# Kernel tuning notes

Measured on AMD Instinct MI355X. Metric: run time of the kernel, lower is better.

## Reference

```python
import jax, jax.numpy as jnp
import numpy as np

R = 2                                   # NMS radius (init kwarg r)
EPS = float(np.finfo(np.float32).eps)   # torch.finfo(float32).eps
PI = float(np.pi)


def _sobel(x):
    """Kornia SpatialGradient (sobel, normalized): x [N,1,H,W] -> (dx, dy) each [N,1,H,W]."""
    kx = jnp.array([[-1., 0., 1.], [-2., 0., 2.], [-1., 0., 1.]], jnp.float32) / 8.0
    ky = kx.T
    k = jnp.stack([kx, ky])[:, None]    # [2,1,3,3] -> out channels dx, dy
    xp = jnp.pad(x, ((0, 0), (0, 0), (1, 1), (1, 1)), mode='edge')  # replicate pad
    out = jax.lax.conv_general_dilated(xp, k, (1, 1), 'VALID',
                                       dimension_numbers=('NCHW', 'OIHW', 'NCHW'))
    return out[:, 0:1], out[:, 1:2]


def _theta(mask):
    """Edge direction from one-hot mask, per STEAL edges_nms. mask [N,1,H,W]."""
    dx, dy = _sobel(mask)
    gxx, _ = _sobel(dx)
    gxy, gyy = _sobel(dy)
    return jnp.fmod(jnp.arctan(gyy * jnp.sign(-gxy + EPS) / (gxx + EPS)), PI)


def setup_inputs() -> dict:
    key = jax.random.key(0)
    k1, k2 = jax.random.split(key)
    pred_labels = jax.random.normal(k1, (4, 16, 512, 1024), dtype=jnp.float32)
    true_labels = jax.random.randint(k2, (4, 512, 1024), 0, 16, dtype=jnp.int64)
    return {"pred_labels": pred_labels, "true_labels": true_labels}


def reference(pred_labels, true_labels):
    B, C, H, W = pred_labels.shape
    # per-class one-hot masks -> direction maps
    onehot = jax.nn.one_hot(true_labels, C, dtype=jnp.float32)        # [B,H,W,C]
    masks = onehot.transpose(0, 3, 1, 2).reshape(B * C, 1, H, W)
    theta = _theta(masks).reshape(B, C, H, W)
    thresh_theta = jnp.fmod(jnp.round(theta * (5.0 / PI)) + 5.0, 5.0)  # {0..4}
    dirs = jnp.fmod(thresh_theta, 4.0).astype(jnp.int32)               # {0,1,2,3}

    exp_p = jnp.exp(pred_labels)
    js = list(range(-R, R))
    # offsets (dx_off, dy_off) summed in the denominator for each direction
    offs = {
        0: [(0, j) for j in js],        # horizontal: preds[x, y-r:y+r]
        1: [(j, -j - 1) for j in js],   # anti-diagonal
        2: [(j, 0) for j in js],        # vertical: preds[x-r:x+r, y]
        3: [(-j - 1, j) for j in js],   # anti-diagonal (reversed traversal, same set)
    }
    denom = jnp.ones_like(exp_p)
    for d in range(4):
        dd = exp_p * 0.0
        for ox, oy in offs[d]:
            dd = dd + jnp.roll(exp_p, (-ox, -oy), axis=(2, 3))  # exp_p[x+ox, y+oy]
        denom = jnp.where(dirs == d, dd, denom)

    interior = jnp.zeros((H, W), bool).at[R:H - R, R:W - R].set(True)
    nms = jnp.where(interior, exp_p / denom, 0.0)
    return jnp.sum(nms)
```

## Files before the change

### kernel.cpp

```cpp
#include <hip/hip_runtime.h>


#define Bn 4
#define Cn 16
#define Hn 512
#define Wn 1024

typedef unsigned long long u64;
typedef unsigned int u32;
typedef float f4u __attribute__((ext_vector_type(4), aligned(4)));
typedef int   i4u __attribute__((ext_vector_type(4), aligned(4)));

static __device__ __forceinline__ float fast_rcp(float x) {
#if __has_builtin(__builtin_amdgcn_rcpf)
  return __builtin_amdgcn_rcpf(x);
#else
  return 1.0f / x;
#endif
}


#define P1TW 128
#define P1TH 8
#define P1LW 132
#define P1LH 12

__global__ __launch_bounds__(256)
void dir_kernel(const int* __restrict__ labels, u32* __restrict__ dirs)
{
  __shared__ unsigned char labt[P1LH][P1LW];

  const int w0 = blockIdx.x * P1TW;
  const int h0 = blockIdx.y * P1TH;
  const int b  = blockIdx.z;
  const int tid = threadIdx.x;

  const int* lbase = labels + (size_t)b * (Hn*Wn);
  const bool interior = (h0 >= 2) && (h0 + P1TH + 2 <= Hn) &&
                        (w0 >= 2) && (w0 + P1TW + 2 <= Wn);
  if (interior) {
    const int* lb = lbase + (size_t)(h0-2)*Wn + (w0-2);
    for (int i = tid; i < P1LH*33; i += 256) {
      int row = i / 33, c4 = (i - row*33) * 4;
      i4u L = *(const i4u*)(lb + row*Wn + c4);
      *(u32*)&labt[row][c4] =
          (u32)L.x | ((u32)L.y << 8) | ((u32)L.z << 16) | ((u32)L.w << 24);
    }
  } else {
    for (int i = tid; i < P1LH*33; i += 256) {
      int row = i / 33, c4 = (i - row*33) * 4;
      int gh = min(max(h0-2+row, 0), Hn-1);
      const int* lr = lbase + gh*Wn;
      u32 v = 0;
      #pragma unroll
      for (int k = 0; k < 4; ++k) {
        int gw = min(max(w0-2+c4+k, 0), Wn-1);
        v |= (u32)(lr[gw] & 0xff) << (8*k);
      }
      *(u32*)&labt[row][c4] = v;
    }
  }
  __syncthreads();

  const int tcol = tid & 31;
  const int trow = tid >> 5;

  u64 W[5];
  #pragma unroll
  for (int r = 0; r < 5; ++r) {
    const u32* lp = (const u32*)&labt[trow + r][0];
    u64 lo = lp[tcol];
    u64 hi = lp[tcol + 1];
    W[r] = lo | (hi << 32);
  }

  u32 pack[4] = {0u, 0u, 0u, 0u};

  #pragma unroll 1
  for (int c = 0; c < 16; ++c) {
    const u64 crep = 0x0101010101010101ULL * (u32)c;
    u64 m[5];
    #pragma unroll
    for (int r = 0; r < 5; ++r) {
      u64 x = W[r] ^ crep;
      m[r] = ((0x8080808080808080ULL - x) & 0x8080808080808080ULL) >> 7;
    }
    u64 t  = m[1] + m[3];
    u64 VA = m[0] + m[4] + (t << 2) + (m[2] << 2) + (m[2] << 1);
    u64 VB = ((m[3] << 1) + m[4] + 0x0303030303030303ULL)
             - (m[0] + (m[1] << 1));
    u64 VC = (m[0] + m[4] + 0x0202020202020202ULL) - (m[2] << 1);
    u64 gxxp = (VA + (VA >> 32) + 0x4040404040404040ULL) - ((VA >> 16) << 1);
    u64 q1   = (VC >> 8) + (VC >> 24);
    u64 w16  = VC >> 16;
    u64 gyyp = (VC + (VC >> 32)) + (q1 << 2) + (w16 << 2) + (w16 << 1);
    u64 gxyp = (((VB >> 24) << 1) + (VB >> 32) + 0x2020202020202020ULL)
             - (VB + ((VB >> 8) << 1));

    u32 gxxl = (u32)gxxp, gyyl = (u32)gyyp, gxyl = (u32)gxyp;
    #pragma unroll
    for (int k = 0; k < 4; ++k) {
      int gxx = (int)((gxxl >> (8*k)) & 0xffu) - 64;
      int gyy = (int)((gyyl >> (8*k)) & 0xffu) - 32;
      int gxyb = (int)((gxyl >> (8*k)) & 0xffu);
      int ax = gxx < 0 ? -gxx : gxx;
      int ay = gyy < 0 ? -gyy : gyy;
      int t1 = (ay * 100  > ax * 33)   ? 1 : 0;
      int t2 = (ay * 1000 > ax * 1377) ? 1 : 0;
      int rb = t1 + t2;
      bool ng = ((gyy < 0) != (gxyb > 32)) != (gxx < 0);
      int dir = ng ? ((rb == 2) ? 3 : 0) : rb;
      pack[k] |= (u32)dir << (2*c);
    }
  }

  const int gh = h0 + trow;
  u32* drow = dirs + ((size_t)b*Hn + gh)*Wn + (w0 + 4*tcol);
  *(uint4*)drow = make_uint4(pack[0], pack[1], pack[2], pack[3]);
}


#define TW 128
#define TH 16
#define LW 132
#define LH 20
#define NT 256

__global__ __launch_bounds__(NT)
void nms_sum_kernel(const float* __restrict__ pred,
                    const u32* __restrict__ dirs,
                    float* __restrict__ slots)
{
  __shared__ float ext[LH][LW];
  __shared__ float wsum[NT/64];

  const int w0 = blockIdx.x * TW;
  const int h0 = blockIdx.y * TH;
  const int bz = blockIdx.z;
  const int b  = bz >> 4;
  const int c  = bz & 15;
  const int tid = threadIdx.x;

  const int lane = tid & 63;
  const int wq   = tid >> 6;
  const int hr0  = wq * 4;
  const int gw0  = w0 + 2*lane;

  u64 dp[4];
  {
    const u32* dbase = dirs + (size_t)b*Hn*Wn;
    #pragma unroll
    for (int i = 0; i < 4; ++i) {
      int gh = h0 + hr0 + i;
      dp[i] = *(const u64*)(dbase + (size_t)gh*Wn + gw0);
    }
  }

  const float* plane = pred + (size_t)(b*Cn + c) * (size_t)(Hn*Wn);
  const bool interior = (h0 >= 2) && (h0 + TH + 2 <= Hn) &&
                        (w0 >= 2) && (w0 + TW + 2 <= Wn);
  if (interior) {
    const float* pb = plane + (size_t)(h0-2)*Wn + (w0-2);
    for (int i = tid; i < LH*33; i += NT) {
      int row = i / 33, c4 = (i - row*33) * 4;
      f4u p = *(const f4u*)(pb + row*Wn + c4);
      float4 e;
      e.x = __expf(p.x); e.y = __expf(p.y); e.z = __expf(p.z); e.w = __expf(p.w);
      *(float4*)&ext[row][c4] = e;
    }
  } else {
    for (int i = tid; i < LH*(LW/2); i += NT) {
      int row = i / (LW/2);
      int col = (i - row*(LW/2)) * 2;
      int gh = min(max(h0-2+row, 0), Hn-1);
      int ga = min(max(w0-2+col,   0), Wn-1);
      int gb = min(max(w0-1+col,   0), Wn-1);
      const float* prow = plane + gh*Wn;
      *(float2*)&ext[row][col] = make_float2(__expf(prow[ga]), __expf(prow[gb]));
    }
  }
  __syncthreads();

  const bool wvalid0 = (gw0     >= 2) && (gw0     < Wn-2);
  const bool wvalid1 = (gw0 + 1 >= 2) && (gw0 + 1 < Wn-2);
  const u32 sh = 2u * (u32)c;

  float acc = 0.f;

  float exr[4][5];
  const int fb = 2*lane;
  #pragma unroll
  for (int r = 0; r < 3; ++r) {
    float2 p0 = *(const float2*)&ext[hr0 + r][fb];
    float2 p1 = *(const float2*)&ext[hr0 + r][fb + 2];
    exr[r][0] = p0.x; exr[r][1] = p0.y;
    exr[r][2] = p1.x; exr[r][3] = p1.y;
    exr[r][4] = ext[hr0 + r][fb + 4];
  }

  #pragma unroll
  for (int i = 0; i < 4; ++i) {
    {
      const int rn = (i + 3) & 3;
      float2 p0 = *(const float2*)&ext[hr0 + i + 3][fb];
      float2 p1 = *(const float2*)&ext[hr0 + i + 3][fb + 2];
      exr[rn][0] = p0.x; exr[rn][1] = p0.y;
      exr[rn][2] = p1.x; exr[rn][3] = p1.y;
      exr[rn][4] = ext[hr0 + i + 3][fb + 4];
    }

    int dir0 = (int)(((u32)dp[i]        >> sh) & 3u);
    int dir1 = (int)(((u32)(dp[i] >> 32) >> sh) & 3u);

    const float* r0 = exr[(i+0)&3];
    const float* r1 = exr[(i+1)&3];
    const float* r2 = exr[(i+2)&3];
    const float* r3 = exr[(i+3)&3];

    float t12 = r2[1] + r2[2];
    float D0a = t12 + r2[0] + r2[3];
    float D0b = t12 + r2[3] + r2[4];
    float D2a = (r0[2] + r1[2]) + (r2[2] + r3[2]);
    float D2b = (r0[3] + r1[3]) + (r2[3] + r3[3]);
    float Dda = (r0[3] + r1[2]) + (r2[1] + r3[0]);
    float Ddb = (r0[4] + r1[3]) + (r2[2] + r3[1]);

    float dena = (dir0 == 0) ? D0a : ((dir0 == 2) ? D2a : Dda);
    float denb = (dir1 == 0) ? D0b : ((dir1 == 2) ? D2b : Ddb);

    const int gh = h0 + hr0 + i;
    const bool hv = (gh >= 2) && (gh < Hn-2);
    float na = (hv && wvalid0) ? r2[2] : 0.f;
    float nb = (hv && wvalid1) ? r2[3] : 0.f;
    acc += na * fast_rcp(dena);
    acc += nb * fast_rcp(denb);
  }

  #pragma unroll
  for (int off = 32; off > 0; off >>= 1)
    acc += __shfl_down(acc, off);
  if (lane == 0) wsum[wq] = acc;
  __syncthreads();
  if (tid == 0) {
    float s = 0.f;
    #pragma unroll
    for (int q = 0; q < NT/64; ++q) s += wsum[q];
    atomicAdd(&slots[(bz << 2) | (blockIdx.x & 3)], s);
  }
}

__global__ __launch_bounds__(64)
void reduce_ws_kernel(const float* __restrict__ slots, float* __restrict__ out)
{
  const int l = threadIdx.x;
  float s = (slots[l] + slots[l + 64]) + (slots[l + 128] + slots[l + 192]);
  #pragma unroll
  for (int off = 32; off > 0; off >>= 1)
    s += __shfl_down(s, off);
  if (l == 0) *out = s;
}

extern "C" void kernel_launch(void* const* d_in, const int* in_sizes, int n_in,
                              void* d_out, int out_size, void* d_ws, size_t ws_size,
                              hipStream_t stream) {
  (void)in_sizes; (void)n_in; (void)ws_size; (void)out_size;
  const float* pred   = (const float*)d_in[0];
  const int*   labels = (const int*)d_in[1];
  float* out = (float*)d_out;

  u32*   dirs  = (u32*)d_ws;
  float* slots = (float*)((char*)d_ws + (size_t)Bn*Hn*Wn*sizeof(u32));

  hipMemsetAsync(slots, 0, 256 * sizeof(float), stream);

  dir_kernel<<<dim3(Wn/P1TW, Hn/P1TH, Bn), 256, 0, stream>>>(labels, dirs);
  nms_sum_kernel<<<dim3(Wn/TW, Hn/TH, Bn*Cn), NT, 0, stream>>>(pred, dirs, slots);
  reduce_ws_kernel<<<1, 64, 0, stream>>>(slots, out);
}
```

Baseline: 263.5 us.

## Double NMS tile height and gather denominator taps via direction-indexed LDS offsets

The NMS kernel tile grows from 16 to 32 rows, so the 2-row halo is a smaller share of each tile and fewer blocks are launched. Each thread now owns one column and 16 rows, reading four direction-selected neighbours from LDS through computed offsets instead of a register sliding window that computed all three candidate sums. This cuts adds but makes LDS reads data-dependent, with more LDS loads per output and possible bank conflicts. The direction kernel also switches its threshold multiplies to __mul24.

New measurement: 247.3 us. 6.2% less time.

```diff
diff --git a/kernel.cpp b/kernel.cpp
--- a/kernel.cpp
+++ b/kernel.cpp
@@ -105,8 +105,8 @@
       int gxyb = (int)((gxyl >> (8*k)) & 0xffu);
       int ax = gxx < 0 ? -gxx : gxx;
       int ay = gyy < 0 ? -gyy : gyy;
-      int t1 = (ay * 100  > ax * 33)   ? 1 : 0;
-      int t2 = (ay * 1000 > ax * 1377) ? 1 : 0;
+      int t1 = (__mul24(ay, 100)  > __mul24(ax, 33))   ? 1 : 0;
+      int t2 = (__mul24(ay, 1000) > __mul24(ax, 1377)) ? 1 : 0;
       int rb = t1 + t2;
       bool ng = ((gyy < 0) != (gxyb > 32)) != (gxx < 0);
       int dir = ng ? ((rb == 2) ? 3 : 0) : rb;
@@ -121,9 +121,9 @@
 
 
 #define TW 128
-#define TH 16
+#define TH 32
 #define LW 132
-#define LH 20
+#define LH 36
 #define NT 256
 
 __global__ __launch_bounds__(NT)
@@ -131,7 +131,7 @@
                     const u32* __restrict__ dirs,
                     float* __restrict__ slots)
 {
-  __shared__ float ext[LH][LW];
+  __shared__ float ext[LH*LW];
   __shared__ float wsum[NT/64];
 
   const int w0 = blockIdx.x * TW;
@@ -141,20 +141,14 @@
   const int c  = bz & 15;
   const int tid = threadIdx.x;
 
-  const int lane = tid & 63;
-  const int wq   = tid >> 6;
-  const int hr0  = wq * 4;
-  const int gw0  = w0 + 2*lane;
-
-  u64 dp[4];
-  {
-    const u32* dbase = dirs + (size_t)b*Hn*Wn;
-    #pragma unroll
-    for (int i = 0; i < 4; ++i) {
-      int gh = h0 + hr0 + i;
-      dp[i] = *(const u64*)(dbase + (size_t)gh*Wn + gw0);
-    }
-  }
+  const int x  = tid & 127;
+  const int rg = tid >> 7;
+  const int gw = w0 + x;
+
+  const u32* dbase = dirs + (size_t)b*Hn*Wn + (size_t)(h0 + rg*16)*Wn + gw;
+  u32 dv[16];
+  #pragma unroll
+  for (int r = 0; r < 16; ++r) dv[r] = dbase[(size_t)r*Wn];
 
   const float* plane = pred + (size_t)(b*Cn + c) * (size_t)(Hn*Wn);
   const bool interior = (h0 >= 2) && (h0 + TH + 2 <= Hn) &&
@@ -166,7 +160,7 @@
       f4u p = *(const f4u*)(pb + row*Wn + c4);
       float4 e;
       e.x = __expf(p.x); e.y = __expf(p.y); e.z = __expf(p.z); e.w = __expf(p.w);
-      *(float4*)&ext[row][c4] = e;
+      *(float4*)&ext[row*LW + c4] = e;
     }
   } else {
     for (int i = tid; i < LH*(LW/2); i += NT) {
@@ -176,66 +170,43 @@
       int ga = min(max(w0-2+col,   0), Wn-1);
       int gb = min(max(w0-1+col,   0), Wn-1);
       const float* prow = plane + gh*Wn;
-      *(float2*)&ext[row][col] = make_float2(__expf(prow[ga]), __expf(prow[gb]));
+      *(float2*)&ext[row*LW+col] = make_float2(__expf(prow[ga]), __expf(prow[gb]));
     }
   }
   __syncthreads();
 
-  const bool wvalid0 = (gw0     >= 2) && (gw0     < Wn-2);
-  const bool wvalid1 = (gw0 + 1 >= 2) && (gw0 + 1 < Wn-2);
+  const bool wv = (gw >= 2) && (gw < Wn-2);
   const u32 sh = 2u * (u32)c;
+  const int ghb = h0 + rg*16;
 
   float acc = 0.f;
-
-  float exr[4][5];
-  const int fb = 2*lane;
-  #pragma unroll
-  for (int r = 0; r < 3; ++r) {
-    float2 p0 = *(const float2*)&ext[hr0 + r][fb];
-    float2 p1 = *(const float2*)&ext[hr0 + r][fb + 2];
-    exr[r][0] = p0.x; exr[r][1] = p0.y;
-    exr[r][2] = p1.x; exr[r][3] = p1.y;
-    exr[r][4] = ext[hr0 + r][fb + 4];
-  }
-
-  #pragma unroll
-  for (int i = 0; i < 4; ++i) {
-    {
-      const int rn = (i + 3) & 3;
-      float2 p0 = *(const float2*)&ext[hr0 + i + 3][fb];
-      float2 p1 = *(const float2*)&ext[hr0 + i + 3][fb + 2];
-      exr[rn][0] = p0.x; exr[rn][1] = p0.y;
-      exr[rn][2] = p1.x; exr[rn][3] = p1.y;
-      exr[rn][4] = ext[hr0 + i + 3][fb + 4];
-    }
-
-    int dir0 = (int)(((u32)dp[i]        >> sh) & 3u);
-    int dir1 = (int)(((u32)(dp[i] >> 32) >> sh) & 3u);
-
-    const float* r0 = exr[(i+0)&3];
-    const float* r1 = exr[(i+1)&3];
-    const float* r2 = exr[(i+2)&3];
-    const float* r3 = exr[(i+3)&3];
-
-    float t12 = r2[1] + r2[2];
-    float D0a = t12 + r2[0] + r2[3];
-    float D0b = t12 + r2[3] + r2[4];
-    float D2a = (r0[2] + r1[2]) + (r2[2] + r3[2]);
-    float D2b = (r0[3] + r1[3]) + (r2[3] + r3[3]);
-    float Dda = (r0[3] + r1[2]) + (r2[1] + r3[0]);
-    float Ddb = (r0[4] + r1[3]) + (r2[2] + r3[1]);
-
-    float dena = (dir0 == 0) ? D0a : ((dir0 == 2) ? D2a : Dda);
-    float denb = (dir1 == 0) ? D0b : ((dir1 == 2) ? D2b : Ddb);
-
-    const int gh = h0 + hr0 + i;
+  const int abase = (rg*16 + 2)*LW + (x + 2);
+
+  #pragma unroll
+  for (int r = 0; r < 16; ++r) {
+    const int a0 = abase + r*LW;
+    const int dir = (int)((dv[r] >> sh) & 3u);
+
+    const int o0 = (dir == 0) ? -2 : ((dir == 2) ? -264 : -263);
+    const int o1 = (dir == 0) ? -1 : -132;
+    const int o2 = -(dir & 1);
+    const int o3 = (dir == 0) ?  1 : ((dir == 2) ?  132 :  130);
+
+    float g0 = ext[a0 + o0];
+    float g1 = ext[a0 + o1];
+    float g2 = ext[a0 + o2];
+    float g3 = ext[a0 + o3];
+    float num = ext[a0];
+    float den = ((g0 + g1) + g2) + g3;
+
+    const int gh = ghb + r;
     const bool hv = (gh >= 2) && (gh < Hn-2);
-    float na = (hv && wvalid0) ? r2[2] : 0.f;
-    float nb = (hv && wvalid1) ? r2[3] : 0.f;
-    acc += na * fast_rcp(dena);
-    acc += nb * fast_rcp(denb);
-  }
-
+    float nn = (hv && wv) ? num : 0.f;
+    acc += nn * fast_rcp(den);
+  }
+
+  const int lane = tid & 63;
+  const int wq   = tid >> 6;
   #pragma unroll
   for (int off = 32; off > 0; off >>= 1)
     acc += __shfl_down(acc, off);
```
